# Kernel optimization log

Measured on AMD Instinct MI355X. Metric: run time of the kernel, lower is better.

The kernel has to match this reference:

```python
import jax, jax.numpy as jnp
import numpy as np

N = 50000      # nodes
E = 800000     # edges (before self-loops)
IN = 128       # in_dim
HID = 64       # hidden_dim
HEADS = 4
OUT = 64       # out_dim
NEG_SLOPE = 0.2
EPS = 1e-16


def gat_conv(x, src, dst, W, att_src, att_dst, b, heads, out_ch, concat):
    """PyG GATConv (eval mode): gather -> attention -> segment softmax -> scatter."""
    n = x.shape[0]
    h = (x @ W).reshape(n, heads, out_ch)                 # [N,H,C]
    a_s = (h * att_src).sum(-1)                           # [N,H]
    a_d = (h * att_dst).sum(-1)                           # [N,H]
    alpha = jax.nn.leaky_relu(a_s[src] + a_d[dst], NEG_SLOPE)   # [E,H]
    amax = jax.ops.segment_max(alpha, dst, num_segments=n)      # stable softmax per dst
    alpha = jnp.exp(alpha - amax[dst])
    denom = jax.ops.segment_sum(alpha, dst, num_segments=n)
    alpha = alpha / (denom[dst] + EPS)
    msg = h[src] * alpha[:, :, None]                      # [E,H,C]
    out = jax.ops.segment_sum(msg, dst, num_segments=n)   # [N,H,C]
    out = out.reshape(n, heads * out_ch) if concat else out.mean(axis=1)
    return out + b


def setup_inputs() -> dict:
    key = jax.random.key(0)
    ks = jax.random.split(key, 16)
    lin = lambda k, fi, fo: jax.random.normal(k, (fi, fo), jnp.float32) / jnp.sqrt(fi)
    x = jax.random.normal(ks[0], (N, IN), jnp.float32)
    edge_index = jax.random.randint(ks[1], (2, E), 0, N, dtype=jnp.int32)
    return {
        "x": x,
        "edge_index": edge_index,
        "W1": lin(ks[2], IN, HEADS * HID),
        "att_src1": jax.random.normal(ks[3], (HEADS, HID)) * 0.1,
        "att_dst1": jax.random.normal(ks[4], (HEADS, HID)) * 0.1,
        "b1": jnp.zeros((HEADS * HID,), jnp.float32),
        "W2": lin(ks[5], HEADS * HID, OUT),
        "att_src2": jax.random.normal(ks[6], (1, OUT)) * 0.1,
        "att_dst2": jax.random.normal(ks[7], (1, OUT)) * 0.1,
        "b2": jnp.zeros((OUT,), jnp.float32),
        "dW1": lin(ks[8], OUT, HID),
        "db1": jnp.zeros((HID,), jnp.float32),
        "dW2": lin(ks[9], HID, IN),
        "db2": jnp.zeros((IN,), jnp.float32),
    }


def reference(x, edge_index, W1, att_src1, att_dst1, b1, W2, att_src2, att_dst2, b2,
              dW1, db1, dW2, db2):
    n = x.shape[0]
    loops = jnp.arange(n, dtype=edge_index.dtype)         # add_self_loops (PyG default)
    src = jnp.concatenate([edge_index[0], loops])
    dst = jnp.concatenate([edge_index[1], loops])
    # encode (dropout is identity in eval mode)
    h = jax.nn.elu(gat_conv(x, src, dst, W1, att_src1, att_dst1, b1, HEADS, HID, True))
    z = gat_conv(h, src, dst, W2, att_src2, att_dst2, b2, 1, OUT, False)
    # F.normalize(z, p=2, dim=-1)
    z = z / jnp.clip(jnp.linalg.norm(z, axis=-1, keepdims=True), 1e-12)
    # feat_decoder: Linear -> ELU -> Linear
    x_hat = jax.nn.elu(z @ dW1 + db1) @ dW2 + db2
    return (z, x_hat)
```

## Files before the change

### kernel.cpp

```cpp
#include <hip/hip_runtime.h>
#include <hip/hip_bf16.h>


#define IN_DIM   128
#define C1       256
#define HEADS    4
#define HID      64
#define OUT_DIM  64

typedef __attribute__((ext_vector_type(8))) short short8;
typedef __attribute__((ext_vector_type(4))) float f32x4;
typedef __attribute__((ext_vector_type(2))) float f32x2;

__device__ __forceinline__ float lrelu(float x) { return x > 0.f ? x : 0.2f * x; }
__device__ __forceinline__ float elu1(float x)  { return x > 0.f ? x : (__expf(x) - 1.f); }
__device__ __forceinline__ float expc(float x)  { return __expf(fminf(x, 60.f)); }
__device__ __forceinline__ float bfu(unsigned int u) {
    union { unsigned int i; float f; } c; c.i = u << 16; return c.f;
}
__device__ __forceinline__ unsigned short pk(float f) {
    union { float f; unsigned int i; } c; c.f = f;
    return (unsigned short)((c.i + 0x7fffu + ((c.i >> 16) & 1u)) >> 16);
}
__device__ __forceinline__ void pkfma_lo(f32x2& acc, const f32x2 x, const f32x2 wp) {
    asm("v_pk_fma_f32 %0, %1, %2, %0 op_sel_hi:[1,0,1]"
        : "+v"(acc) : "v"(x), "v"(wp));
}
__device__ __forceinline__ void pkfma_hi(f32x2& acc, const f32x2 x, const f32x2 wp) {
    asm("v_pk_fma_f32 %0, %1, %2, %0 op_sel:[0,1,0] op_sel_hi:[1,1,1]"
        : "+v"(acc) : "v"(x), "v"(wp));
}
__device__ __forceinline__ f32x2 bf2up(unsigned int u) {
    union { unsigned int i[2]; f32x2 f; } c;
    c.i[0] = u << 16;
    c.i[1] = u & 0xffff0000u;
    return c.f;
}

__global__ __launch_bounds__(256) void w1f_k(const float* __restrict__ W1,
                                             const float* __restrict__ W2,
                                             const float* __restrict__ as1,
                                             const float* __restrict__ ad1,
                                             unsigned short* __restrict__ W1f,
                                             unsigned short* __restrict__ W2f,
                                             float* __restrict__ u_s,
                                             float* __restrict__ u_d)
{
    const int b = blockIdx.x;
    if (b == 16) {
        for (int idx = threadIdx.x; idx < 512; idx += 256) {
            const int h = idx >> 7, k = idx & 127;
            float ss = 0.f, dd = 0.f;
            #pragma unroll 4
            for (int c = 0; c < 64; ++c) {
                const float wv = W1[k * 256 + h * 64 + c];
                ss += wv * as1[h * 64 + c];
                dd += wv * ad1[h * 64 + c];
            }
            u_s[idx] = ss;
            u_d[idx] = dd;
        }
        return;
    }
    if (b >= 17) {
        const int idx = (b - 17) * 256 + threadIdx.x;
        if (idx >= 32 * 64) return;
        const int lane = idx & 63, e = idx >> 6;
        const int nt = e >> 3, kc = e & 7, q = lane >> 4, c = lane & 15;
        unsigned short tmp[8];
        #pragma unroll
        for (int j = 0; j < 8; ++j)
            tmp[j] = pk(W2[(kc * 32 + q * 8 + j) * 64 + nt * 16 + c]);
        ushort4* dst = (ushort4*)(W2f + (size_t)idx * 8);
        dst[0] = make_ushort4(tmp[0], tmp[1], tmp[2], tmp[3]);
        dst[1] = make_ushort4(tmp[4], tmp[5], tmp[6], tmp[7]);
        return;
    }
    const int idx = b * 256 + threadIdx.x;
    if (idx >= 64 * 64) return;
    const int lane = idx & 63, e = idx >> 6;
    const int nt = e >> 2, kc = e & 3, q = lane >> 4, c = lane & 15;
    unsigned short tmp[8];
    #pragma unroll
    for (int j = 0; j < 8; ++j)
        tmp[j] = pk(W1[(kc * 32 + q * 8 + j) * 256 + nt * 16 + c]);
    ushort4* dst = (ushort4*)(W1f + (size_t)idx * 8);
    dst[0] = make_ushort4(tmp[0], tmp[1], tmp[2], tmp[3]);
    dst[1] = make_ushort4(tmp[4], tmp[5], tmp[6], tmp[7]);
}

__global__ __launch_bounds__(256) void xprep_deg_k(
    const float* __restrict__ x, const float* __restrict__ u_s,
    const float* __restrict__ u_d, unsigned short* __restrict__ xb,
    float* __restrict__ a_s1, float* __restrict__ a_d1, int N,
    const int* __restrict__ ei, int E, int Etot, int* __restrict__ rowptr,
    int dgrid)
{
    if (blockIdx.x < dgrid) {
        const int per = (Etot + dgrid - 1) / dgrid;
        const int e0 = blockIdx.x * per, e1 = min(e0 + per, Etot);
        for (int e = e0 + threadIdx.x; e < e1; e += 256) {
            const int d = (e < E) ? ei[E + e] : e - E;
            atomicAdd(&rowptr[1 + d], 1);
        }
        return;
    }
    __shared__ float us[512], ud[512];
    const int t = threadIdx.x;
    for (int i = t; i < 512; i += 256) { us[i] = u_s[i]; ud[i] = u_d[i]; }
    __syncthreads();
    const int w = t >> 6, l = t & 63;
    const int n = (blockIdx.x - dgrid) * 4 + w;
    if (n >= N) return;
    const float2 xv = *(const float2*)&x[(size_t)n * IN_DIM + 2 * l];
    const unsigned int p2 =
        (unsigned int)pk(xv.x) | ((unsigned int)pk(xv.y) << 16);
    *(unsigned int*)&xb[(size_t)n * IN_DIM + 2 * l] = p2;
    #pragma unroll
    for (int h = 0; h < 4; ++h) {
        float ps = xv.x * us[h * 128 + 2 * l] + xv.y * us[h * 128 + 2 * l + 1];
        float pd = xv.x * ud[h * 128 + 2 * l] + xv.y * ud[h * 128 + 2 * l + 1];
        #pragma unroll
        for (int off = 1; off < 64; off <<= 1) {
            ps += __shfl_xor(ps, off, 64);
            pd += __shfl_xor(pd, off, 64);
        }
        if (l == 0) {
            a_s1[n * 4 + h] = ps;
            a_d1[n * 4 + h] = pd;
        }
    }
}

__device__ __forceinline__ int blk_incl_scan(int v, int t) {
    __shared__ int wsum[4];
    const int lane = t & 63, wid = t >> 6;
    int s = v;
    #pragma unroll
    for (int off = 1; off < 64; off <<= 1) {
        const int u = __shfl_up(s, off, 64);
        if (lane >= off) s += u;
    }
    if (lane == 63) wsum[wid] = s;
    __syncthreads();
    int add = 0;
    #pragma unroll
    for (int k = 0; k < 4; ++k) if (k < wid) add += wsum[k];
    __syncthreads();
    return s + add;
}

__global__ __launch_bounds__(256) void scanA_k(const int* __restrict__ rowptr,
                                               int* __restrict__ psum, int N)
{
    const int t = threadIdx.x;
    const int i = blockIdx.x * 256 + t;
    int v = (i < N) ? rowptr[1 + i] : 0;
    #pragma unroll
    for (int off = 1; off < 64; off <<= 1) v += __shfl_xor(v, off, 64);
    __shared__ int ws[4];
    if ((t & 63) == 0) ws[t >> 6] = v;
    __syncthreads();
    if (t == 0) psum[blockIdx.x] = ws[0] + ws[1] + ws[2] + ws[3];
}

__global__ __launch_bounds__(256) void scanC_k(int* __restrict__ rowptr,
                                               int* __restrict__ cursor,
                                               const int* __restrict__ psum,
                                               int N, int SC)
{
    const int t = threadIdx.x;
    int s = (t < SC && t < (int)blockIdx.x) ? psum[t] : 0;
    #pragma unroll
    for (int off = 1; off < 64; off <<= 1) s += __shfl_xor(s, off, 64);
    __shared__ int bsum[4];
    if ((t & 63) == 0) bsum[t >> 6] = s;
    __syncthreads();
    const int base = bsum[0] + bsum[1] + bsum[2] + bsum[3];
    __syncthreads();
    const int i = blockIdx.x * 256 + t;
    const int v = (i < N) ? rowptr[1 + i] : 0;
    const int inc = blk_incl_scan(v, t);
    if (i < N) {
        rowptr[1 + i] = base + inc;
        cursor[i]     = base + inc - v;
    }
}

__global__ __launch_bounds__(256) void fill_k(const int* __restrict__ ei, int E,
                                              int Etot, int* __restrict__ cursor,
                                              int* __restrict__ col, int N)
{
    const int bin = blockIdx.x & 7;
    const int chunk = blockIdx.x >> 3, nchunk = gridDim.x >> 3;
    const int per = (Etot + nchunk - 1) / nchunk;
    const int e0 = chunk * per, e1 = min(e0 + per, Etot);
    const int lo = (int)(((long long)N * bin) >> 3);
    const int hi = (int)(((long long)N * (bin + 1)) >> 3);
    for (int e = e0 + threadIdx.x; e < e1; e += 256) {
        const int d = (e < E) ? ei[E + e] : e - E;
        if (d >= lo && d < hi) {
            const int s = (e < E) ? ei[e] : d;
            const int pos = atomicAdd(&cursor[d], 1);
            col[pos] = s;
        }
    }
}

__global__ __launch_bounds__(256) void agg1x_k(
    const int* __restrict__ rowptr, const int* __restrict__ col,
    const float* __restrict__ a_s1, const float* __restrict__ a_d1,
    const unsigned short* __restrict__ xb, unsigned short* __restrict__ xagg,
    int N)
{
    __shared__ int    scolS[4][64];
    __shared__ float4 w4S[4][64];
    const int t = threadIdx.x, w = t >> 6, l = t & 63;
    const int n = blockIdx.x * 4 + w;
    if (n >= N) return;
    const int beg = rowptr[n], end = rowptr[n + 1];
    const float4 dv = *(const float4*)&a_d1[n * 4];
    float4 ws = {0.f, 0.f, 0.f, 0.f};
    f32x2 acc[4] = {{0.f,0.f},{0.f,0.f},{0.f,0.f},{0.f,0.f}};
    const unsigned short* xbl = xb + 2 * l;
    for (int t0 = beg; t0 < end; t0 += 64) {
        const int m = min(64, end - t0);
        const int p = t0 + l;
        int sc = 0;
        float4 wv = {0.f, 0.f, 0.f, 0.f};
        if (p < end) {
            sc = col[p];
            const float4 av = *(const float4*)&a_s1[sc * 4];
            wv.x = expc(lrelu(av.x + dv.x));
            wv.y = expc(lrelu(av.y + dv.y));
            wv.z = expc(lrelu(av.z + dv.z));
            wv.w = expc(lrelu(av.w + dv.w));
            ws.x += wv.x; ws.y += wv.y; ws.z += wv.z; ws.w += wv.w;
        }
        scolS[w][l] = sc;
        w4S[w][l]   = wv;
        __threadfence_block();
        for (int j0 = 0; j0 < m; j0 += 8) {
            const int4 s0 = *(const int4*)&scolS[w][j0];
            const int4 s1 = *(const int4*)&scolS[w][j0 + 4];
            const int su[8] = {s0.x, s0.y, s0.z, s0.w, s1.x, s1.y, s1.z, s1.w};
            unsigned int hv[8];
            #pragma unroll
            for (int u = 0; u < 8; ++u)
                hv[u] = *(const unsigned int*)(xbl + (size_t)su[u] * IN_DIM);
            #pragma unroll
            for (int u = 0; u < 8; ++u) {
                const float* wb = (const float*)&w4S[w][j0 + u];
                const f32x2 wp01 = *(const f32x2*)(wb);
                const f32x2 wp23 = *(const f32x2*)(wb + 2);
                const f32x2 xv = bf2up(hv[u]);
                pkfma_lo(acc[0], xv, wp01);
                pkfma_hi(acc[1], xv, wp01);
                pkfma_lo(acc[2], xv, wp23);
                pkfma_hi(acc[3], xv, wp23);
            }
        }
    }
    #pragma unroll
    for (int off = 1; off < 64; off <<= 1) {
        ws.x += __shfl_xor(ws.x, off, 64);
        ws.y += __shfl_xor(ws.y, off, 64);
        ws.z += __shfl_xor(ws.z, off, 64);
        ws.w += __shfl_xor(ws.w, off, 64);
    }
    const float i0 = 1.f / (ws.x + 1e-16f), i1 = 1.f / (ws.y + 1e-16f);
    const float i2 = 1.f / (ws.z + 1e-16f), i3 = 1.f / (ws.w + 1e-16f);
    unsigned short* out = xagg + (size_t)n * 512 + 2 * l;
    *(unsigned int*)(out)       = (unsigned int)pk(acc[0][0] * i0) |
                                  ((unsigned int)pk(acc[0][1] * i0) << 16);
    *(unsigned int*)(out + 128) = (unsigned int)pk(acc[1][0] * i1) |
                                  ((unsigned int)pk(acc[1][1] * i1) << 16);
    *(unsigned int*)(out + 256) = (unsigned int)pk(acc[2][0] * i2) |
                                  ((unsigned int)pk(acc[2][1] * i2) << 16);
    *(unsigned int*)(out + 384) = (unsigned int)pk(acc[3][0] * i3) |
                                  ((unsigned int)pk(acc[3][1] * i3) << 16);
}

__global__ __launch_bounds__(256) void gemm12_k(
    const unsigned short* __restrict__ xagg, const unsigned short* __restrict__ W1f,
    const float* __restrict__ b1, const unsigned short* __restrict__ W2f,
    const float* __restrict__ as2, const float* __restrict__ ad2,
    unsigned short* __restrict__ h2b, float* __restrict__ a_s2,
    float* __restrict__ a_d2, int N)
{
    __shared__ short lds[64 * 264];
    const int t = threadIdx.x, w = t >> 6, l = t & 63;
    const int q = l >> 4, c = l & 15;
    const int n0 = blockIdx.x * 64;
    const int arow = 16 * w + c;
    f32x4 acc[16];
    #pragma unroll
    for (int nt = 0; nt < 16; ++nt) acc[nt] = (f32x4){0.f, 0.f, 0.f, 0.f};
    #pragma unroll
    for (int half = 0; half < 2; ++half) {
        if (half) __syncthreads();
        for (int i = t; i < 64 * 32; i += 256) {
            const int r = i >> 5, ch = (i & 31) * 8;
            const int rn = min(n0 + r, N - 1);
            *(short8*)&lds[r * 264 + ch] =
                *(const short8*)&xagg[(size_t)rn * 512 + half * 256 + ch];
        }
        __syncthreads();
        #pragma unroll
        for (int hh = 0; hh < 2; ++hh) {
            const int h = half * 2 + hh;
            short8 afr[4];
            #pragma unroll
            for (int kc = 0; kc < 4; ++kc)
                afr[kc] = *(const short8*)&lds[arow * 264 + hh * 128 + kc * 32 + q * 8];
            #pragma unroll
            for (int nt = 0; nt < 4; ++nt) {
                #pragma unroll
                for (int kc = 0; kc < 4; ++kc) {
                    const short8 bfr = *(const short8*)(W1f +
                        ((size_t)((h * 4 + nt) * 4 + kc) * 64 + l) * 8);
                    acc[h * 4 + nt] = __builtin_amdgcn_mfma_f32_16x16x32_bf16(
                        afr[kc], bfr, acc[h * 4 + nt], 0, 0, 0);
                }
            }
        }
    }
    __syncthreads();
    #pragma unroll
    for (int nt = 0; nt < 16; ++nt)
        #pragma unroll
        for (int r = 0; r < 4; ++r) {
            const float v = elu1(acc[nt][r] + b1[nt * 16 + c]);
            lds[(16 * w + q * 4 + r) * 264 + nt * 16 + c] = (short)pk(v);
        }
    __syncthreads();
    short8 afr2[8];
    #pragma unroll
    for (int kc = 0; kc < 8; ++kc)
        afr2[kc] = *(const short8*)&lds[arow * 264 + kc * 32 + q * 8];
    f32x4 acc2[4];
    #pragma unroll
    for (int nt = 0; nt < 4; ++nt) acc2[nt] = (f32x4){0.f, 0.f, 0.f, 0.f};
    #pragma unroll
    for (int nt = 0; nt < 4; ++nt) {
        #pragma unroll
        for (int kc = 0; kc < 8; ++kc) {
            const short8 bfr =
                *(const short8*)(W2f + ((size_t)(nt * 8 + kc) * 64 + l) * 8);
            acc2[nt] = __builtin_amdgcn_mfma_f32_16x16x32_bf16(afr2[kc], bfr,
                                                               acc2[nt], 0, 0, 0);
        }
    }
    {
        float vsr[4] = {0.f, 0.f, 0.f, 0.f}, vdr[4] = {0.f, 0.f, 0.f, 0.f};
        #pragma unroll
        for (int nt = 0; nt < 4; ++nt) {
            const float sa = as2[nt * 16 + c], da = ad2[nt * 16 + c];
            #pragma unroll
            for (int r = 0; r < 4; ++r) {
                vsr[r] += acc2[nt][r] * sa;
                vdr[r] += acc2[nt][r] * da;
            }
        }
        #pragma unroll
        for (int r = 0; r < 4; ++r) {
            #pragma unroll
            for (int off = 1; off < 16; off <<= 1) {
                vsr[r] += __shfl_xor(vsr[r], off, 64);
                vdr[r] += __shfl_xor(vdr[r], off, 64);
            }
            const int node = n0 + 16 * w + q * 4 + r;
            if (c == 0 && node < N) {
                a_s2[node] = vsr[r];
                a_d2[node] = vdr[r];
            }
        }
    }
    __syncthreads();
    #pragma unroll
    for (int nt = 0; nt < 4; ++nt)
        #pragma unroll
        for (int r = 0; r < 4; ++r)
            lds[(16 * w + q * 4 + r) * 72 + nt * 16 + c] = (short)pk(acc2[nt][r]);
    __syncthreads();
    for (int i = t; i < 64 * 8; i += 256) {
        const int r = i >> 3, ch = (i & 7) * 8;
        const int node = n0 + r;
        if (node < N)
            *(short8*)&h2b[(size_t)node * OUT_DIM + ch] =
                *(const short8*)&lds[r * 72 + ch];
    }
}

__global__ __launch_bounds__(256) void agg2_k(
    const int* __restrict__ rowptr, const int* __restrict__ col,
    const float* __restrict__ a_s2, const float* __restrict__ a_d2,
    const unsigned short* __restrict__ h2b, const float* __restrict__ b2,
    float* __restrict__ zout, int N)
{
    __shared__ int2 swS[4][64];
    const int t = threadIdx.x, w = t >> 6, l = t & 63;
    const int n = blockIdx.x * 4 + w;
    if (n >= N) return;
    const int beg = rowptr[n], end = rowptr[n + 1];
    const float dn = a_d2[n];
    const int half = l >> 5, c2 = l & 31;
    f32x2 acc = {0.f, 0.f};
    float wsum = 0.f;
    const unsigned short* h2l = h2b + 2 * c2;
    for (int t0 = beg; t0 < end; t0 += 64) {
        const int m = min(64, end - t0);
        const int p = t0 + l;
        int sc = 0; float wv = 0.f;
        if (p < end) {
            sc = col[p];
            wv = expc(lrelu(a_s2[sc] + dn));
            wsum += wv;
        }
        swS[w][l] = make_int2(sc, __float_as_int(wv));
        __threadfence_block();
        const int pairs = (m + 1) >> 1;
        for (int j0 = 0; j0 < pairs; j0 += 8) {
            int2 sv[8];
            #pragma unroll
            for (int u = 0; u < 8; ++u)
                sv[u] = swS[w][2 * (j0 + u) + half];
            unsigned int hv[8];
            #pragma unroll
            for (int u = 0; u < 8; ++u)
                hv[u] = *(const unsigned int*)(h2l + (size_t)sv[u].x * OUT_DIM);
            #pragma unroll
            for (int u = 0; u < 8; ++u) {
                union { int2 i; f32x2 f; } cv; cv.i = sv[u];
                pkfma_hi(acc, bf2up(hv[u]), cv.f);
            }
        }
    }
    float a0 = acc[0], a1 = acc[1];
    a0 += __shfl_xor(a0, 32, 64);
    a1 += __shfl_xor(a1, 32, 64);
    #pragma unroll
    for (int off = 1; off < 64; off <<= 1) wsum += __shfl_xor(wsum, off, 64);
    const float inv = 1.f / (wsum + 1e-16f);
    float z0 = a0 * inv + b2[2 * c2];
    float z1 = a1 * inv + b2[2 * c2 + 1];
    float sq = z0 * z0 + z1 * z1;
    #pragma unroll
    for (int off = 1; off < 32; off <<= 1) sq += __shfl_xor(sq, off, 64);
    const float rn = 1.f / fmaxf(sqrtf(sq), 1e-12f);
    if (l < 32) {
        float2 o; o.x = z0 * rn; o.y = z1 * rn;
        *(float2*)&zout[(size_t)n * OUT_DIM + 2 * c2] = o;
    }
}

__global__ __launch_bounds__(256) void dec_k(
    const float* __restrict__ z,
    const float* __restrict__ dW1, const float* __restrict__ db1,
    const float* __restrict__ dW2, const float* __restrict__ db2,
    float* __restrict__ xhat, int N)
{
    __shared__ float zs[32 * 64];
    __shared__ float ts[32 * 64];
    const int t = threadIdx.x;
    const int n0 = blockIdx.x * 32;
    for (int i = t; i < 32 * 64; i += 256) {
        const int nb_l = i >> 6, k = i & 63;
        const int n = min(n0 + nb_l, N - 1);
        zs[(nb_l >> 3) * 512 + k * 8 + (nb_l & 7)] = z[(size_t)n * OUT_DIM + k];
    }
    __syncthreads();
    const int w = t >> 6, l = t & 63;
    const float* zw = zs + w * 512;
    float* tw = ts + w * 512;
    float acc[8] = {0.f, 0.f, 0.f, 0.f, 0.f, 0.f, 0.f, 0.f};
    #pragma unroll 4
    for (int k = 0; k < 64; ++k) {
        const float wv = dW1[k * HID + l];
        const float4 xa = *(const float4*)&zw[k * 8];
        const float4 xb = *(const float4*)&zw[k * 8 + 4];
        acc[0] += xa.x * wv; acc[1] += xa.y * wv;
        acc[2] += xa.z * wv; acc[3] += xa.w * wv;
        acc[4] += xb.x * wv; acc[5] += xb.y * wv;
        acc[6] += xb.z * wv; acc[7] += xb.w * wv;
    }
    const float bb = db1[l];
    #pragma unroll
    for (int nb = 0; nb < 8; ++nb) tw[l * 8 + nb] = elu1(acc[nb] + bb);
    __syncthreads();
    float a0[8] = {0.f, 0.f, 0.f, 0.f, 0.f, 0.f, 0.f, 0.f};
    float a1[8] = {0.f, 0.f, 0.f, 0.f, 0.f, 0.f, 0.f, 0.f};
    #pragma unroll 2
    for (int k = 0; k < 64; ++k) {
        const float w0 = dW2[k * IN_DIM + l];
        const float w1 = dW2[k * IN_DIM + 64 + l];
        const float4 xa = *(const float4*)&tw[k * 8];
        const float4 xb = *(const float4*)&tw[k * 8 + 4];
        const float xv[8] = {xa.x, xa.y, xa.z, xa.w, xb.x, xb.y, xb.z, xb.w};
        #pragma unroll
        for (int nb = 0; nb < 8; ++nb) {
            a0[nb] += xv[nb] * w0;
            a1[nb] += xv[nb] * w1;
        }
    }
    const float bb0 = db2[l], bb1 = db2[64 + l];
    #pragma unroll
    for (int nb = 0; nb < 8; ++nb) {
        const int n = n0 + w * 8 + nb;
        if (n >= N) break;
        xhat[(size_t)n * IN_DIM + l]      = a0[nb] + bb0;
        xhat[(size_t)n * IN_DIM + 64 + l] = a1[nb] + bb1;
    }
}

extern "C" void kernel_launch(void* const* d_in, const int* in_sizes, int n_in,
                              void* d_out, int out_size, void* d_ws, size_t ws_size,
                              hipStream_t stream)
{
    const float* x   = (const float*)d_in[0];
    const int*   ei  = (const int*)d_in[1];
    const float* W1  = (const float*)d_in[2];
    const float* as1 = (const float*)d_in[3];
    const float* ad1 = (const float*)d_in[4];
    const float* b1  = (const float*)d_in[5];
    const float* W2  = (const float*)d_in[6];
    const float* as2 = (const float*)d_in[7];
    const float* ad2 = (const float*)d_in[8];
    const float* b2  = (const float*)d_in[9];
    const float* dW1 = (const float*)d_in[10];
    const float* db1 = (const float*)d_in[11];
    const float* dW2 = (const float*)d_in[12];
    const float* db2 = (const float*)d_in[13];

    const int N    = in_sizes[0] / IN_DIM;
    const int E    = in_sizes[1] / 2;
    const int Etot = E + N;

    unsigned short* W1f = (unsigned short*)d_ws;
    unsigned short* W2f = W1f + 32768;
    float* u_s = (float*)(W2f + 16384);
    float* u_d = u_s + 512;
    unsigned short* xagg = (unsigned short*)(u_d + 512);
    unsigned short* xb   = xagg + (size_t)N * 512;
    unsigned short* h2b  = xb   + (size_t)N * IN_DIM;
    float* a_s1 = (float*)(h2b + (size_t)N * OUT_DIM);
    float* a_d1 = a_s1 + (size_t)N * HEADS;
    float* a_s2 = a_d1 + (size_t)N * HEADS;
    float* a_d2 = a_s2 + (size_t)N;
    int* rowptr = (int*)(a_d2 + (size_t)N);
    int* cursor = rowptr + (N + 1);
    int* col    = cursor + N;
    int* psum   = col + Etot;

    const size_t needed = (size_t)N * 1456 + (size_t)Etot * 4 + 103432;
    if (ws_size < needed) return;

    hipMemsetAsync(rowptr, 0, (size_t)(N + 1) * sizeof(int), stream);

    const int SC    = (N + 255) / 256;
    const int mblk  = (N + 63) / 64;
    const int nblk4 = (N + 3) / 4;
    const int nchunk = (Etot + 2047) / 2048;
    const int bgrid  = nchunk * 8;
    w1f_k     <<<25, 256, 0, stream>>>(W1, W2, as1, ad1, W1f, W2f, u_s, u_d);
    xprep_deg_k<<<nchunk + nblk4, 256, 0, stream>>>(x, u_s, u_d, xb, a_s1,
                                                    a_d1, N, ei, E, Etot,
                                                    rowptr, nchunk);
    scanA_k   <<<SC, 256, 0, stream>>>(rowptr, psum, N);
    scanC_k   <<<SC, 256, 0, stream>>>(rowptr, cursor, psum, N, SC);
    fill_k    <<<bgrid, 256, 0, stream>>>(ei, E, Etot, cursor, col, N);
    agg1x_k   <<<nblk4, 256, 0, stream>>>(rowptr, col, a_s1, a_d1, xb, xagg, N);
    gemm12_k  <<<mblk, 256, 0, stream>>>(xagg, W1f, b1, W2f, as2, ad2, h2b,
                                         a_s2, a_d2, N);
    agg2_k    <<<nblk4, 256, 0, stream>>>(rowptr, col, a_s2, a_d2, h2b, b2,
                                          (float*)d_out, N);
    dec_k     <<<(N + 31) / 32, 256, 0, stream>>>((const float*)d_out, dW1, db1,
                                                  dW2, db2,
                                                  (float*)d_out + (size_t)N * OUT_DIM, N);
}
```

Measured before the change: 336.9 us.

## Build CSR via two-level radix bucketing instead of global per-node atomics

Replaces the per-node global-atomic degree count, two-pass scan and binned fill with a two-level counting sort. Edges are first bucketed by dst>>8 using shared-memory histograms into an intermediate buffer of packed (src, low dst byte) words. Each 256-node bucket is then locally sorted in one block to produce rowptr and col. This is meant to cut global atomic contention and the scattered writes of the old fill. In exchange it needs an extra Etot-sized buffer and a second pass over the edges, and it assumes N fits in 256 buckets and that src fits in 24 bits.

```diff
diff --git a/kernel.cpp b/kernel.cpp
--- a/kernel.cpp
+++ b/kernel.cpp
@@ -89,20 +89,27 @@
     dst[1] = make_ushort4(tmp[4], tmp[5], tmp[6], tmp[7]);
 }
 
-__global__ __launch_bounds__(256) void xprep_deg_k(
+__global__ __launch_bounds__(256) void xprep_cnt_k(
     const float* __restrict__ x, const float* __restrict__ u_s,
     const float* __restrict__ u_d, unsigned short* __restrict__ xb,
     float* __restrict__ a_s1, float* __restrict__ a_d1, int N,
-    const int* __restrict__ ei, int E, int Etot, int* __restrict__ rowptr,
-    int dgrid)
-{
-    if (blockIdx.x < dgrid) {
-        const int per = (Etot + dgrid - 1) / dgrid;
+    const int* __restrict__ ei, int E, int Etot, int* __restrict__ rtot,
+    int CA, int NR)
+{
+    if (blockIdx.x < CA) {
+        __shared__ int hist[256];
+        const int t = threadIdx.x;
+        for (int i = t; i < NR; i += 256) hist[i] = 0;
+        __syncthreads();
+        const int per = (Etot + CA - 1) / CA;
         const int e0 = blockIdx.x * per, e1 = min(e0 + per, Etot);
-        for (int e = e0 + threadIdx.x; e < e1; e += 256) {
+        for (int e = e0 + t; e < e1; e += 256) {
             const int d = (e < E) ? ei[E + e] : e - E;
-            atomicAdd(&rowptr[1 + d], 1);
-        }
+            atomicAdd(&hist[d >> 8], 1);
+        }
+        __syncthreads();
+        for (int i = t; i < NR; i += 256)
+            if (hist[i]) atomicAdd(&rtot[i], hist[i]);
         return;
     }
     __shared__ float us[512], ud[512];
@@ -110,7 +117,7 @@
     for (int i = t; i < 512; i += 256) { us[i] = u_s[i]; ud[i] = u_d[i]; }
     __syncthreads();
     const int w = t >> 6, l = t & 63;
-    const int n = (blockIdx.x - dgrid) * 4 + w;
+    const int n = (blockIdx.x - CA) * 4 + w;
     if (n >= N) return;
     const float2 xv = *(const float2*)&x[(size_t)n * IN_DIM + 2 * l];
     const unsigned int p2 =
@@ -150,60 +157,80 @@
     return s + add;
 }
 
-__global__ __launch_bounds__(256) void scanA_k(const int* __restrict__ rowptr,
-                                               int* __restrict__ psum, int N)
+__global__ __launch_bounds__(256) void scanR_k(const int* __restrict__ rtot,
+                                               int* __restrict__ rbase,
+                                               int* __restrict__ rcur,
+                                               int* __restrict__ rowptr,
+                                               int NR, int N, int Etot)
 {
     const int t = threadIdx.x;
-    const int i = blockIdx.x * 256 + t;
-    int v = (i < N) ? rowptr[1 + i] : 0;
-    #pragma unroll
-    for (int off = 1; off < 64; off <<= 1) v += __shfl_xor(v, off, 64);
-    __shared__ int ws[4];
-    if ((t & 63) == 0) ws[t >> 6] = v;
-    __syncthreads();
-    if (t == 0) psum[blockIdx.x] = ws[0] + ws[1] + ws[2] + ws[3];
-}
-
-__global__ __launch_bounds__(256) void scanC_k(int* __restrict__ rowptr,
-                                               int* __restrict__ cursor,
-                                               const int* __restrict__ psum,
-                                               int N, int SC)
-{
+    const int v = (t < NR) ? rtot[t] : 0;
+    const int inc = blk_incl_scan(v, t);
+    if (t < NR) {
+        rbase[t] = inc - v;
+        rcur[t]  = inc - v;
+    }
+    if (t == 0) rowptr[N] = Etot;
+}
+
+__global__ __launch_bounds__(256) void scat_k(const int* __restrict__ ei,
+                                              int E, int Etot,
+                                              int* __restrict__ rcur,
+                                              unsigned int* __restrict__ eb,
+                                              int CA, int NR)
+{
+    __shared__ int hist[256], base[256];
     const int t = threadIdx.x;
-    int s = (t < SC && t < (int)blockIdx.x) ? psum[t] : 0;
-    #pragma unroll
-    for (int off = 1; off < 64; off <<= 1) s += __shfl_xor(s, off, 64);
-    __shared__ int bsum[4];
-    if ((t & 63) == 0) bsum[t >> 6] = s;
-    __syncthreads();
-    const int base = bsum[0] + bsum[1] + bsum[2] + bsum[3];
-    __syncthreads();
-    const int i = blockIdx.x * 256 + t;
-    const int v = (i < N) ? rowptr[1 + i] : 0;
+    for (int i = t; i < NR; i += 256) hist[i] = 0;
+    __syncthreads();
+    const int per = (Etot + CA - 1) / CA;
+    const int e0 = blockIdx.x * per, e1 = min(e0 + per, Etot);
+    for (int e = e0 + t; e < e1; e += 256) {
+        const int d = (e < E) ? ei[E + e] : e - E;
+        atomicAdd(&hist[d >> 8], 1);
+    }
+    __syncthreads();
+    for (int i = t; i < NR; i += 256) {
+        base[i] = hist[i] ? atomicAdd(&rcur[i], hist[i]) : 0;
+        hist[i] = 0;
+    }
+    __syncthreads();
+    for (int e = e0 + t; e < e1; e += 256) {
+        int s, d;
+        if (e < E) { s = ei[e]; d = ei[E + e]; } else { s = d = e - E; }
+        const int r = d >> 8;
+        const int local = atomicAdd(&hist[r], 1);
+        eb[base[r] + local] = (unsigned int)s | ((unsigned int)(d & 255) << 24);
+    }
+}
+
+__global__ __launch_bounds__(256) void rsort_k(const unsigned int* __restrict__ eb,
+                                               const int* __restrict__ rtot,
+                                               const int* __restrict__ rbase,
+                                               int* __restrict__ rowptr,
+                                               int* __restrict__ col, int N)
+{
+    __shared__ int hist[256], off[256];
+    const int r = blockIdx.x;
+    const int t = threadIdx.x;
+    hist[t] = 0;
+    __syncthreads();
+    const int e0 = rbase[r], cnt = rtot[r];
+    for (int i = t; i < cnt; i += 256)
+        atomicAdd(&hist[eb[e0 + i] >> 24], 1);
+    __syncthreads();
+    const int v = hist[t];
     const int inc = blk_incl_scan(v, t);
-    if (i < N) {
-        rowptr[1 + i] = base + inc;
-        cursor[i]     = base + inc - v;
-    }
-}
-
-__global__ __launch_bounds__(256) void fill_k(const int* __restrict__ ei, int E,
-                                              int Etot, int* __restrict__ cursor,
-                                              int* __restrict__ col, int N)
-{
-    const int bin = blockIdx.x & 7;
-    const int chunk = blockIdx.x >> 3, nchunk = gridDim.x >> 3;
-    const int per = (Etot + nchunk - 1) / nchunk;
-    const int e0 = chunk * per, e1 = min(e0 + per, Etot);
-    const int lo = (int)(((long long)N * bin) >> 3);
-    const int hi = (int)(((long long)N * (bin + 1)) >> 3);
-    for (int e = e0 + threadIdx.x; e < e1; e += 256) {
-        const int d = (e < E) ? ei[E + e] : e - E;
-        if (d >= lo && d < hi) {
-            const int s = (e < E) ? ei[e] : d;
-            const int pos = atomicAdd(&cursor[d], 1);
-            col[pos] = s;
-        }
+    off[t] = inc - v;
+    const int node = r * 256 + t;
+    if (node < N) rowptr[node] = e0 + off[t];
+    hist[t] = 0;
+    __syncthreads();
+    for (int i = t; i < cnt; i += 256) {
+        const unsigned int ev = eb[e0 + i];
+        const int ld = ev >> 24;
+        const int local = atomicAdd(&hist[ld], 1);
+        col[e0 + off[ld] + local] = (int)(ev & 0xFFFFFFu);
     }
 }
 
@@ -535,6 +562,7 @@
     const int N    = in_sizes[0] / IN_DIM;
     const int E    = in_sizes[1] / 2;
     const int Etot = E + N;
+    const int NR   = (N + 255) >> 8;
 
     unsigned short* W1f = (unsigned short*)d_ws;
     unsigned short* W2f = W1f + 32768;
@@ -548,33 +576,32 @@
     float* a_s2 = a_d1 + (size_t)N * HEADS;
     float* a_d2 = a_s2 + (size_t)N;
     int* rowptr = (int*)(a_d2 + (size_t)N);
-    int* cursor = rowptr + (N + 1);
-    int* col    = cursor + N;
-    int* psum   = col + Etot;
-
-    const size_t needed = (size_t)N * 1456 + (size_t)Etot * 4 + 103432;
-    if (ws_size < needed) return;
-
-    hipMemsetAsync(rowptr, 0, (size_t)(N + 1) * sizeof(int), stream);
-
-    const int SC    = (N + 255) / 256;
+    int* col    = rowptr + (N + 1);
+    unsigned int* eb = (unsigned int*)(col + Etot);
+    int* rtot   = (int*)(eb + Etot);
+    int* rbase  = rtot + 256;
+    int* rcur   = rbase + 256;
+
+    const size_t needed = (size_t)N * 1452 + (size_t)Etot * 8 + 105512;
+    if (ws_size < needed || NR > 256) return;
+
+    hipMemsetAsync(rtot, 0, 256 * sizeof(int), stream);
+
     const int mblk  = (N + 63) / 64;
     const int nblk4 = (N + 3) / 4;
-    const int nchunk = (Etot + 2047) / 2048;
-    const int bgrid  = nchunk * 8;
-    w1f_k     <<<25, 256, 0, stream>>>(W1, W2, as1, ad1, W1f, W2f, u_s, u_d);
-    xprep_deg_k<<<nchunk + nblk4, 256, 0, stream>>>(x, u_s, u_d, xb, a_s1,
-                                                    a_d1, N, ei, E, Etot,
-                                                    rowptr, nchunk);
-    scanA_k   <<<SC, 256, 0, stream>>>(rowptr, psum, N);
-    scanC_k   <<<SC, 256, 0, stream>>>(rowptr, cursor, psum, N, SC);
-    fill_k    <<<bgrid, 256, 0, stream>>>(ei, E, Etot, cursor, col, N);
-    agg1x_k   <<<nblk4, 256, 0, stream>>>(rowptr, col, a_s1, a_d1, xb, xagg, N);
-    gemm12_k  <<<mblk, 256, 0, stream>>>(xagg, W1f, b1, W2f, as2, ad2, h2b,
-                                         a_s2, a_d2, N);
-    agg2_k    <<<nblk4, 256, 0, stream>>>(rowptr, col, a_s2, a_d2, h2b, b2,
-                                          (float*)d_out, N);
-    dec_k     <<<(N + 31) / 32, 256, 0, stream>>>((const float*)d_out, dW1, db1,
-                                                  dW2, db2,
-                                                  (float*)d_out + (size_t)N * OUT_DIM, N);
-}
+    const int CA    = (Etot + 2047) / 2048;
+    w1f_k      <<<25, 256, 0, stream>>>(W1, W2, as1, ad1, W1f, W2f, u_s, u_d);
+    xprep_cnt_k<<<CA + nblk4, 256, 0, stream>>>(x, u_s, u_d, xb, a_s1, a_d1,
+                                                N, ei, E, Etot, rtot, CA, NR);
+    scanR_k    <<<1, 256, 0, stream>>>(rtot, rbase, rcur, rowptr, NR, N, Etot);
+    scat_k     <<<CA, 256, 0, stream>>>(ei, E, Etot, rcur, eb, CA, NR);
+    rsort_k    <<<NR, 256, 0, stream>>>(eb, rtot, rbase, rowptr, col, N);
+    agg1x_k    <<<nblk4, 256, 0, stream>>>(rowptr, col, a_s1, a_d1, xb, xagg, N);
+    gemm12_k   <<<mblk, 256, 0, stream>>>(xagg, W1f, b1, W2f, as2, ad2, h2b,
+                                          a_s2, a_d2, N);
+    agg2_k     <<<nblk4, 256, 0, stream>>>(rowptr, col, a_s2, a_d2, h2b, b2,
+                                           (float*)d_out, N);
+    dec_k      <<<(N + 31) / 32, 256, 0, stream>>>((const float*)d_out, dW1,
+                                                   db1, dW2, db2,
+                                                   (float*)d_out + (size_t)N * OUT_DIM, N);
+}
```

Measured after the change: 310.9 us. -7.7%, faster.
